# Kernel tuning notes

Hardware: AMD Instinct MI355X
Metric: run time of the kernel (lower is better)

The kernel has to match this reference:

```python
import jax, jax.numpy as jnp
import numpy as np

B, T, C, HS = 8, 4096, 1024, 128
BLOCK = 4096  # block_size; T == BLOCK here


def _pyr_mask(bs):
    # Faithful numpy translation of the torch 'pyr' buffer construction.
    h = bs // 2
    top = np.repeat(np.flip(np.tril(np.ones((h, h), np.float32)), axis=1), 2, axis=0)  # (bs, h)
    reps = np.array([2] * (h - 1) + [1])
    bot = np.concatenate(
        [np.zeros((1, h), np.float32),
         np.repeat(np.tril(np.ones((h, h), np.float32)), reps, axis=0)], axis=0)  # (bs, h)
    return np.concatenate([top, bot], axis=1)  # (bs, bs)


def setup_inputs() -> dict:
    key = jax.random.key(0)
    kx, kq, kk, kv = jax.random.split(key, 4)
    s = C ** -0.5
    x = jax.random.normal(kx, (B, T, C), jnp.float32)
    Wq = jax.random.normal(kq, (C, HS), jnp.float32) * s
    Wk = jax.random.normal(kk, (C, HS), jnp.float32) * s
    Wv = jax.random.normal(kv, (C, HS), jnp.float32) * s
    return {"x": x, "Wq": Wq, "Wk": Wk, "Wv": Wv}


def reference(x, Wq, Wk, Wv):
    Tlen = x.shape[1]
    start = (BLOCK - Tlen) // 2
    end = BLOCK + (-(BLOCK - Tlen)) // 2  # python floor-div, matches torch slicing
    mask = jnp.asarray(_pyr_mask(BLOCK)[:Tlen, start:end])  # (T, T) 0/1

    q = x @ Wq  # (B, T, HS)
    k = x @ Wk
    v = x @ Wv
    wei = jnp.einsum('btd,bsd->bts', q, k) * (HS ** -0.5)  # (B, T, T)
    wei = jnp.where(mask == 0, -jnp.inf, wei)  # bidirectional_mode == 'bi'
    wei = jax.nn.softmax(wei, axis=-1)
    # dropout p=0.0 -> identity
    return wei @ v  # (B, T, HS)
```

## Files before the change

kernel.cpp:

```cpp
#include <hip/hip_runtime.h>

typedef unsigned short u16;
typedef __attribute__((ext_vector_type(8))) short bf16x8;
typedef __attribute__((ext_vector_type(8))) unsigned short u16x8;
typedef __attribute__((ext_vector_type(4))) float f32x4;
typedef __attribute__((ext_vector_type(4))) unsigned short u16x4;
typedef __attribute__((ext_vector_type(2))) unsigned int u32x2;
typedef __attribute__((ext_vector_type(4))) unsigned int u32x4;

#define Bn 8
#define Tn 4096
#define Cn 1024
#define HSn 128

#define SBAR __builtin_amdgcn_sched_barrier(0)

__device__ __forceinline__ float bf2f(u16 b) {
    unsigned u = ((unsigned)b) << 16;
    return __builtin_bit_cast(float, u);
}
__device__ __forceinline__ unsigned cvt_pk_bf16(float a, float b) {
    unsigned r;
    asm("v_cvt_pk_bf16_f32 %0, %1, %2" : "=v"(r) : "v"(a), "v"(b));
    return r;
}
__device__ __forceinline__ u16 f2bf(float f) { return (u16)cvt_pk_bf16(f, f); }

__device__ __forceinline__ void wg_barrier() {
    __builtin_amdgcn_sched_barrier(0);
    asm volatile("s_waitcnt lgkmcnt(0)" ::: "memory");
    __builtin_amdgcn_s_barrier();
    __builtin_amdgcn_sched_barrier(0);
}

__device__ __forceinline__ void dma16(const void* g, void* l) {
    __builtin_amdgcn_global_load_lds(
        (const __attribute__((address_space(1))) unsigned int*)g,
        (__attribute__((address_space(3))) unsigned int*)l, 16, 0, 0);
}

extern "C" __global__ __launch_bounds__(256) void head_wtrans(
    const float* __restrict__ Wq, const float* __restrict__ Wk,
    const float* __restrict__ Wv, u16* __restrict__ wt) {
    const float* W = (blockIdx.y == 0) ? Wq : (blockIdx.y == 1) ? Wk : Wv;
    const float scale =
        (blockIdx.y == 0) ? (0.08838834764831845f * 1.4426950408889634f) : 1.0f;
    u16* o = wt + (size_t)blockIdx.y * Cn * HSn;
    int tid = blockIdx.x * 256 + threadIdx.x;
    int n = tid >> 10, kk = tid & 1023;
    o[tid] = f2bf(W[kk * HSn + n] * scale);
}

extern "C" __global__ __launch_bounds__(256) void head_proj(
    const float* __restrict__ x, const u16* __restrict__ wt, u16* __restrict__ qo,
    u16* __restrict__ ko, u16* __restrict__ vto) {
    __shared__ __align__(16) unsigned char sh[3 * 8192];
    const int tid = threadIdx.x;
    const int w = tid >> 6, l = tid & 63, quad = l >> 4, ln = l & 15;
    const int bm0 = blockIdx.x * 64;
    const int n0 = w * 96;

    const f32x4 zero4 = {0.f, 0.f, 0.f, 0.f};
    f32x4 acc[4][6];
#pragma unroll
    for (int fi = 0; fi < 4; fi++)
#pragma unroll
        for (int ci = 0; ci < 6; ci++) acc[fi][ci] = zero4;

    const float* xg[2];
    int xd[2];
#pragma unroll
    for (int p = 0; p < 2; p++) {
        int s = p * 256 + tid;
        int row = s >> 3, slot = s & 7;
        int g = slot ^ (row & 7);
        xg[p] = x + (size_t)(bm0 + row) * Cn + g * 4;
        xd[p] = s * 16;
    }
    int aoff[4];
#pragma unroll
    for (int fi = 0; fi < 4; fi++) {
        int row = fi * 16 + ln;
        aoff[fi] = row * 128 + (((2 * quad) ^ (row & 7)) * 16);
    }
    const u16* bp[6];
#pragma unroll
    for (int ci = 0; ci < 6; ci++)
        bp[ci] = wt + (size_t)(n0 + ci * 16 + ln) * Cn + quad * 8;

#define P_DMA(BUF, KT)                                       \
    do {                                                     \
        dma16(xg[0] + (KT) * 32, sh + (BUF) * 8192 + xd[0]); \
        dma16(xg[1] + (KT) * 32, sh + (BUF) * 8192 + xd[1]); \
    } while (0)

#define P_LOADB(DST, KT)                                   \
    do {                                                   \
        _Pragma("unroll") for (int ci = 0; ci < 6; ci++)   \
            DST[ci] = *(const u16x8*)(bp[ci] + (KT) * 32); \
    } while (0)

#define P_COMPUTE(BUF, BREG)                                               \
    do {                                                                   \
        const unsigned char* cb = sh + (BUF) * 8192;                       \
        bf16x8 af[4];                                                      \
        _Pragma("unroll") for (int fi = 0; fi < 4; fi++) {                 \
            f32x4 lo = *(const f32x4*)(cb + aoff[fi]);                     \
            f32x4 hi = *(const f32x4*)(cb + (aoff[fi] ^ 16));              \
            u32x4 tt;                                                      \
            tt[0] = cvt_pk_bf16(lo[0], lo[1]);                             \
            tt[1] = cvt_pk_bf16(lo[2], lo[3]);                             \
            tt[2] = cvt_pk_bf16(hi[0], hi[1]);                             \
            tt[3] = cvt_pk_bf16(hi[2], hi[3]);                             \
            af[fi] = __builtin_bit_cast(bf16x8, tt);                       \
        }                                                                  \
        _Pragma("unroll") for (int ci = 0; ci < 6; ci++) {                 \
            bf16x8 bfr = __builtin_bit_cast(bf16x8, BREG[ci]);             \
            _Pragma("unroll") for (int fi = 0; fi < 4; fi++)               \
                acc[fi][ci] = __builtin_amdgcn_mfma_f32_16x16x32_bf16(     \
                    af[fi], bfr, acc[fi][ci], 0, 0, 0);                    \
        }                                                                  \
    } while (0)

#define P_PHASE(T, BUF, BCUR, BNXT)                                         \
    do {                                                                    \
        int t_ = (T);                                                       \
        if (t_ < 32) {                                                      \
            P_COMPUTE(BUF, BCUR);                                           \
            wg_barrier();                                                   \
            if (t_ + 2 < 32) P_LOADB(BNXT, t_ + 2);                         \
            if (t_ + 3 < 32) P_DMA(BUF, t_ + 3);                            \
            SBAR;                                                           \
            if (t_ <= 28)                                                   \
                asm volatile("s_waitcnt vmcnt(16)" ::: "memory");           \
            else if (t_ == 29)                                              \
                asm volatile("s_waitcnt vmcnt(14)" ::: "memory");           \
            else if (t_ == 30)                                              \
                asm volatile("s_waitcnt vmcnt(6)" ::: "memory");            \
            if (t_ < 31) __builtin_amdgcn_s_barrier();                      \
            SBAR;                                                           \
        }                                                                   \
    } while (0)

    u16x8 b0[6], b1[6], b2[6];
    P_DMA(0, 0);
    P_LOADB(b0, 0);
    P_DMA(1, 1);
    P_LOADB(b1, 1);
    P_DMA(2, 2);
    SBAR;
    asm volatile("s_waitcnt vmcnt(16)" ::: "memory");
    __builtin_amdgcn_s_barrier();
    SBAR;

    for (int t3 = 0; t3 < 33; t3 += 3) {
        P_PHASE(t3 + 0, 0, b0, b2);
        P_PHASE(t3 + 1, 1, b1, b0);
        P_PHASE(t3 + 2, 2, b2, b1);
    }
#undef P_DMA
#undef P_LOADB
#undef P_COMPUTE
#undef P_PHASE

    u16* const tL = (u16*)sh;
#pragma unroll
    for (int ci = 0; ci < 6; ci++) {
        int col = n0 + ci * 16 + ln;
        int cin = col & 127;
        int sidx = col >> 7;
#pragma unroll
        for (int fi = 0; fi < 4; fi++) {
            int grow = bm0 + fi * 16 + quad * 4;
            if (sidx == 0) {
#pragma unroll
                for (int r = 0; r < 4; r++)
                    qo[(size_t)(grow + r) * HSn + cin] = f2bf(acc[fi][ci][r]);
            } else if (sidx == 1) {
#pragma unroll
                for (int r = 0; r < 4; r++)
                    ko[(size_t)(grow + r) * HSn + cin] = f2bf(acc[fi][ci][r]);
            } else {
                u16x4 pk4;
#pragma unroll
                for (int r = 0; r < 4; r++) pk4[r] = f2bf(acc[fi][ci][r]);
                *(u16x4*)(tL + cin * 80 + (fi * 16 + quad * 4)) = pk4;
            }
        }
    }
    wg_barrier();
    {
        const int bb = bm0 >> 12, t0b = bm0 & 4095;
        const int dl = tid >> 3, tch = (tid & 7) * 8;
#pragma unroll
        for (int dp = 0; dp < 4; dp++) {
            int d = dp * 32 + dl;
            u16x8 vv = *(const u16x8*)(tL + d * 80 + tch);
            *(u16x8*)(vto + ((size_t)bb * HSn + d) * Tn + t0b + tch) = vv;
        }
    }
}

extern "C" __global__ __launch_bounds__(512) void head_flash_chunk(
    const u16* __restrict__ q, const u16* __restrict__ k, const u16* __restrict__ vt,
    u16* __restrict__ Opart, float* __restrict__ lsum) {
    __shared__ __align__(16) u16 kL[64 * 136];
    __shared__ __align__(16) u16 vL[128 * 72];
    __shared__ __align__(16) u16 pL[8 * 16 * 72];
    const int tid = threadIdx.x;
    const int w = tid >> 6, l = tid & 63, quad = l >> 4, ln = l & 15;
    const int cid = blockIdx.x;
    const int grp = cid >> 4;
    const int qbi = (grp < 16) ? (31 - grp) : (grp - 16);
    const int b = (cid >> 1) & 7;
    const int half = cid & 1;
    const int q0 = qbi * 128;
    const int qrow = q0 + w * 16;

    const int rkBase = tid >> 4, ckK = tid & 15;
    const int rvBase = tid >> 3, ckV = tid & 7;

    bf16x8 qf[4];
#pragma unroll
    for (int ks = 0; ks < 4; ks++)
        qf[ks] = *(const bf16x8*)(q + ((size_t)b * Tn + qrow + ln) * HSn + ks * 32 +
                                  quad * 8);

    const f32x4 zero4 = {0.f, 0.f, 0.f, 0.f};
    float l2 = 0.f;
    const int qme = qrow + ln;
    const int clo = 2047 - (qme >> 1), chi = 2047 + ((qme + 1) >> 1);
    const int cloW0 = 2047 - (qrow >> 1);
    const int chiW0 = 2047 + ((qrow + 1) >> 1);
    const int cloMin = 2047 - ((qrow + 15) >> 1);
    const int chiMax = 2047 + ((qrow + 16) >> 1);
    f32x4 o[8];
#pragma unroll
    for (int dt = 0; dt < 8; dt++) o[dt] = zero4;

    const int qmax = q0 + 127;
    const int tlo = (2047 - (qmax >> 1)) >> 6;
    const int thi = (2047 + ((qmax + 1) >> 1)) >> 6;
    const int W = thi - tlo + 1;
    const int c0 = (W + 1) >> 1;
    const int kstart = half ? tlo + c0 : tlo;
    const int kend = half ? thi : tlo + c0 - 1;

    u16x8 pk[2], pv[2];
    {
        const int t0 = kstart * 64;
#pragma unroll
        for (int p = 0; p < 2; p++)
            pk[p] = *(const u16x8*)(k + ((size_t)b * Tn + t0 + p * 32 + rkBase) * HSn +
                                    ckK * 8);
#pragma unroll
        for (int p = 0; p < 2; p++)
            pv[p] = *(const u16x8*)(vt + ((size_t)b * HSn + p * 64 + rvBase) * Tn + t0 +
                                    ckV * 8);
    }

    for (int kt = kstart; kt <= kend; kt++) {
        const int t0 = kt * 64;
        wg_barrier();
#pragma unroll
        for (int p = 0; p < 2; p++)
            *(u16x8*)(kL + (p * 32 + rkBase) * 136 + ckK * 8) = pk[p];
#pragma unroll
        for (int p = 0; p < 2; p++)
            *(u16x8*)(vL + (p * 64 + rvBase) * 72 + ckV * 8) = pv[p];
        if (kt < kend) {
            const int t1 = t0 + 64;
#pragma unroll
            for (int p = 0; p < 2; p++)
                pk[p] = *(const u16x8*)(k + ((size_t)b * Tn + t1 + p * 32 + rkBase) * HSn +
                                        ckK * 8);
#pragma unroll
            for (int p = 0; p < 2; p++)
                pv[p] = *(const u16x8*)(vt + ((size_t)b * HSn + p * 64 + rvBase) * Tn +
                                        t1 + ckV * 8);
        }
        wg_barrier();

        const bool live = !((t0 + 63 < cloMin) || (t0 > chiMax));

        if (live) {
            f32x4 s[4];
#pragma unroll
            for (int nt = 0; nt < 4; nt++) s[nt] = zero4;
            __builtin_amdgcn_s_setprio(1);
#pragma unroll
            for (int nt = 0; nt < 4; nt++) {
                int R = nt * 16 + ln;
#pragma unroll
                for (int ks = 0; ks < 4; ks++) {
                    bf16x8 kf = *(const bf16x8*)(kL + R * 136 + (ks * 4 + quad) * 8);
                    s[nt] =
                        __builtin_amdgcn_mfma_f32_16x16x32_bf16(kf, qf[ks], s[nt], 0, 0, 0);
                }
            }
            __builtin_amdgcn_s_setprio(0);
            if (t0 < cloW0 || t0 + 63 > chiW0) {
#pragma unroll
                for (int nt = 0; nt < 4; nt++)
#pragma unroll
                    for (int r = 0; r < 4; r++) {
                        int t = t0 + nt * 16 + quad * 4 + r;
                        bool valid = (t >= clo) && (t <= chi);
                        s[nt][r] = valid ? s[nt][r] : -1e30f;
                    }
            }
            float ls = 0.f;
#pragma unroll
            for (int nt = 0; nt < 4; nt++) {
                float p0 = exp2f(s[nt][0]), p1 = exp2f(s[nt][1]);
                float p2 = exp2f(s[nt][2]), p3 = exp2f(s[nt][3]);
                ls += (p0 + p1) + (p2 + p3);
                u32x2 d;
                d.x = cvt_pk_bf16(p0, p1);
                d.y = cvt_pk_bf16(p2, p3);
                *(u32x2*)(pL + w * 1152 + ln * 72 + nt * 16 + quad * 4) = d;
            }
            l2 += ls;
            __builtin_amdgcn_s_setprio(1);
#pragma unroll
            for (int jt = 0; jt < 2; jt++) {
                bf16x8 pf = *(const bf16x8*)(pL + w * 1152 + ln * 72 + jt * 32 + quad * 8);
#pragma unroll
                for (int dt = 0; dt < 8; dt++) {
                    int R = dt * 16 + ln;
                    bf16x8 vf = *(const bf16x8*)(vL + R * 72 + (jt * 4 + quad) * 8);
                    o[dt] = __builtin_amdgcn_mfma_f32_16x16x32_bf16(pf, vf, o[dt], 0, 0, 0);
                }
            }
            __builtin_amdgcn_s_setprio(0);
        }
    }
    l2 += __shfl_xor(l2, 16, 64);
    l2 += __shfl_xor(l2, 32, 64);
#pragma unroll
    for (int dt = 0; dt < 8; dt++)
#pragma unroll
        for (int r = 0; r < 4; r++)
            Opart[((size_t)cid * 128 + w * 16 + quad * 4 + r) * HSn + dt * 16 + ln] =
                f2bf(o[dt][r]);
    if (l < 16) lsum[(size_t)cid * 128 + w * 16 + ln] = l2;
}

extern "C" __global__ __launch_bounds__(256) void head_combine(
    const u16* __restrict__ Opart, const float* __restrict__ lsum,
    float* __restrict__ out) {
    const int bid = blockIdx.x;
    const int qb64 = bid >> 3, b = bid & 7;
    const int tid = threadIdx.x;
    const int row = tid >> 2, dseg = (tid & 3) * 32;
    const int qbi = qb64 >> 1;
    const int inrow = (qb64 & 1) * 64 + row;
    const int grp0 = (qbi >= 16) ? (31 - qbi) : (qbi + 16);
    const int cid0 = grp0 * 16 + b * 2;
    const size_t r0 = (size_t)cid0 * 128 + inrow, r1 = r0 + 128;
    float l0 = lsum[r0], l1 = lsum[r1];
    float inv = 1.0f / (l0 + l1);
    float* op = out + ((size_t)b * Tn + qb64 * 64 + row) * HSn + dseg;
    const u16* p0 = Opart + r0 * HSn + dseg;
    const u16* p1 = Opart + r1 * HSn + dseg;
#pragma unroll
    for (int j = 0; j < 4; j++) {
        u16x8 a = *(const u16x8*)(p0 + j * 8);
        u16x8 c = *(const u16x8*)(p1 + j * 8);
        f32x4 o1, o2;
#pragma unroll
        for (int e = 0; e < 4; e++) o1[e] = (bf2f(a[e]) + bf2f(c[e])) * inv;
#pragma unroll
        for (int e = 0; e < 4; e++) o2[e] = (bf2f(a[4 + e]) + bf2f(c[4 + e])) * inv;
        *(f32x4*)(op + j * 8) = o1;
        *(f32x4*)(op + j * 8 + 4) = o2;
    }
}

extern "C" __global__ __launch_bounds__(256) void head_flash(
    const u16* __restrict__ q, const u16* __restrict__ k, const u16* __restrict__ vt,
    float* __restrict__ out) {
    __shared__ __align__(16) u16 kL[64 * 136];
    __shared__ __align__(16) u16 vL[128 * 72];
    __shared__ __align__(16) u16 pL[4 * 16 * 72];
    const int tid = threadIdx.x;
    const int w = tid >> 6, l = tid & 63, quad = l >> 4, ln = l & 15;
    const int bx = blockIdx.x;
    const int half = bx >> 8, idx = bx & 255;
    const int p5 = idx & 31, b = idx >> 5;
    const int qb = half ? p5 : 63 - p5;
    const int q0 = qb * 64;
    const int qrow = q0 + w * 16;
    const int rkBase = tid >> 4, ckK = tid & 15;
    const int rvBase = tid >> 3, ckV = tid & 7;

    bf16x8 qf[4];
#pragma unroll
    for (int ks = 0; ks < 4; ks++)
        qf[ks] = *(const bf16x8*)(q + ((size_t)b * Tn + qrow + ln) * HSn + ks * 32 +
                                  quad * 8);
    const f32x4 zero4 = {0.f, 0.f, 0.f, 0.f};
    float m2 = -1e30f, l2 = 0.f;
    const int qme = qrow + ln;
    const int clo = 2047 - (qme >> 1), chi = 2047 + ((qme + 1) >> 1);
    f32x4 o[8];
#pragma unroll
    for (int dt = 0; dt < 8; dt++) o[dt] = zero4;
    const int qmax = q0 + 63;
    const int tlo = (2047 - (qmax >> 1)) >> 6;
    const int thi = (2047 + ((qmax + 1) >> 1)) >> 6;

    u16x8 pk[4], pv[4];
    {
        const int t0 = tlo * 64;
#pragma unroll
        for (int p = 0; p < 4; p++)
            pk[p] = *(const u16x8*)(k + ((size_t)b * Tn + t0 + p * 16 + rkBase) * HSn +
                                    ckK * 8);
#pragma unroll
        for (int p = 0; p < 4; p++)
            pv[p] = *(const u16x8*)(vt + ((size_t)b * HSn + p * 32 + rvBase) * Tn + t0 +
                                    ckV * 8);
    }
    for (int kt = tlo; kt <= thi; kt++) {
        const int t0 = kt * 64;
        __syncthreads();
#pragma unroll
        for (int p = 0; p < 4; p++)
            *(u16x8*)(kL + (p * 16 + rkBase) * 136 + ckK * 8) = pk[p];
#pragma unroll
        for (int p = 0; p < 4; p++)
            *(u16x8*)(vL + (p * 32 + rvBase) * 72 + ckV * 8) = pv[p];
        if (kt < thi) {
            const int t1 = t0 + 64;
#pragma unroll
            for (int p = 0; p < 4; p++)
                pk[p] = *(const u16x8*)(k + ((size_t)b * Tn + t1 + p * 16 + rkBase) * HSn +
                                        ckK * 8);
#pragma unroll
            for (int p = 0; p < 4; p++)
                pv[p] = *(const u16x8*)(vt + ((size_t)b * HSn + p * 32 + rvBase) * Tn +
                                        t1 + ckV * 8);
        }
        __syncthreads();
        f32x4 s[4];
#pragma unroll
        for (int nt = 0; nt < 4; nt++) s[nt] = zero4;
#pragma unroll
        for (int nt = 0; nt < 4; nt++) {
            int R = nt * 16 + ln;
#pragma unroll
            for (int ks = 0; ks < 4; ks++) {
                bf16x8 kf = *(const bf16x8*)(kL + R * 136 + (ks * 4 + quad) * 8);
                s[nt] = __builtin_amdgcn_mfma_f32_16x16x32_bf16(kf, qf[ks], s[nt], 0, 0, 0);
            }
        }
#pragma unroll
        for (int nt = 0; nt < 4; nt++)
#pragma unroll
            for (int r = 0; r < 4; r++) {
                int t = t0 + nt * 16 + quad * 4 + r;
                bool valid = (t >= clo) && (t <= chi);
                s[nt][r] = valid ? s[nt][r] : -1e30f;
            }
        float mc = s[0][0];
#pragma unroll
        for (int nt = 0; nt < 4; nt++)
#pragma unroll
            for (int r = 0; r < 4; r++) mc = fmaxf(mc, s[nt][r]);
        mc = fmaxf(mc, __shfl_xor(mc, 16, 64));
        mc = fmaxf(mc, __shfl_xor(mc, 32, 64));
        float mn = fmaxf(m2, mc);
        float alpha = exp2f(m2 - mn);
        m2 = mn;
        float ls = 0.f;
#pragma unroll
        for (int nt = 0; nt < 4; nt++) {
            float p0 = exp2f(s[nt][0] - mn), p1 = exp2f(s[nt][1] - mn);
            float p2 = exp2f(s[nt][2] - mn), p3 = exp2f(s[nt][3] - mn);
            ls += (p0 + p1) + (p2 + p3);
            u32x2 d;
            d.x = cvt_pk_bf16(p0, p1);
            d.y = cvt_pk_bf16(p2, p3);
            *(u32x2*)(pL + w * 1152 + ln * 72 + nt * 16 + quad * 4) = d;
        }
        ls += __shfl_xor(ls, 16, 64);
        ls += __shfl_xor(ls, 32, 64);
        l2 = l2 * alpha + ls;
        float aR[4];
#pragma unroll
        for (int r = 0; r < 4; r++) aR[r] = __shfl(alpha, quad * 4 + r, 64);
#pragma unroll
        for (int dt = 0; dt < 8; dt++) {
            f32x4 oo = o[dt];
#pragma unroll
            for (int r = 0; r < 4; r++) oo[r] *= aR[r];
            o[dt] = oo;
        }
#pragma unroll
        for (int jt = 0; jt < 2; jt++) {
            bf16x8 pf = *(const bf16x8*)(pL + w * 1152 + ln * 72 + jt * 32 + quad * 8);
#pragma unroll
            for (int dt = 0; dt < 8; dt++) {
                int R = dt * 16 + ln;
                bf16x8 vf = *(const bf16x8*)(vL + R * 72 + (jt * 4 + quad) * 8);
                o[dt] = __builtin_amdgcn_mfma_f32_16x16x32_bf16(pf, vf, o[dt], 0, 0, 0);
            }
        }
    }
    float inv = 1.0f / l2;
    float rl[4];
#pragma unroll
    for (int r = 0; r < 4; r++) rl[r] = __shfl(inv, quad * 4 + r, 64);
#pragma unroll
    for (int dt = 0; dt < 8; dt++)
#pragma unroll
        for (int r = 0; r < 4; r++) {
            int row = qrow + quad * 4 + r;
            out[((size_t)b * Tn + row) * HSn + dt * 16 + ln] = o[dt][r] * rl[r];
        }
}

extern "C" void kernel_launch(void* const* d_in, const int* in_sizes, int n_in,
                              void* d_out, int out_size, void* d_ws, size_t ws_size,
                              hipStream_t stream) {
    const float* x = (const float*)d_in[0];
    const float* Wq = (const float*)d_in[1];
    const float* Wk = (const float*)d_in[2];
    const float* Wv = (const float*)d_in[3];
    float* outp = (float*)d_out;
    char* ws = (char*)d_ws;
    u16* wt = (u16*)(ws);
    u16* qb = (u16*)(ws + (1u << 20));
    u16* kb = (u16*)(ws + (9u << 20));
    u16* vtb = (u16*)(ws + (17u << 20));
    u16* Opart = (u16*)(ws + (25u << 20));
    float* lsum = (float*)(ws + (42u << 20));

    head_wtrans<<<dim3(512, 3), 256, 0, stream>>>(Wq, Wk, Wv, wt);
    head_proj<<<dim3(512), 256, 0, stream>>>(x, wt, qb, kb, vtb);
    if (ws_size >= (44ull << 20)) {
        head_flash_chunk<<<dim3(512), 512, 0, stream>>>(qb, kb, vtb, Opart, lsum);
        head_combine<<<dim3(512), 256, 0, stream>>>(Opart, lsum, outp);
    } else {
        head_flash<<<dim3(512), 256, 0, stream>>>(qb, kb, vtb, outp);
    }
}
```

Measured before the change: 310.5 us.

## Restructure projection GEMM pipeline to double buffering with asm loads and setprio

```diff
diff --git a/kernel.cpp b/kernel.cpp
--- a/kernel.cpp
+++ b/kernel.cpp
@@ -25,6 +25,12 @@
     return r;
 }
 __device__ __forceinline__ u16 f2bf(float f) { return (u16)cvt_pk_bf16(f, f); }
+
+__device__ __forceinline__ u32x4 gld16(const u16* p) {
+    u32x4 d;
+    asm volatile("global_load_dwordx4 %0, %1, off" : "=&v"(d) : "v"(p));
+    return d;
+}
 
 __device__ __forceinline__ void wg_barrier() {
     __builtin_amdgcn_sched_barrier(0);
@@ -54,7 +60,7 @@
 extern "C" __global__ __launch_bounds__(256) void head_proj(
     const float* __restrict__ x, const u16* __restrict__ wt, u16* __restrict__ qo,
     u16* __restrict__ ko, u16* __restrict__ vto) {
-    __shared__ __align__(16) unsigned char sh[3 * 8192];
+    __shared__ __align__(16) unsigned char sh[20480];
     const int tid = threadIdx.x;
     const int w = tid >> 6, l = tid & 63, quad = l >> 4, ln = l & 15;
     const int bm0 = blockIdx.x * 64;
@@ -94,10 +100,10 @@
         dma16(xg[1] + (KT) * 32, sh + (BUF) * 8192 + xd[1]); \
     } while (0)
 
-#define P_LOADB(DST, KT)                                   \
-    do {                                                   \
-        _Pragma("unroll") for (int ci = 0; ci < 6; ci++)   \
-            DST[ci] = *(const u16x8*)(bp[ci] + (KT) * 32); \
+#define P_LOADB(DST, KT)                                 \
+    do {                                                 \
+        _Pragma("unroll") for (int ci = 0; ci < 6; ci++) \
+            DST[ci] = gld16(bp[ci] + (KT) * 32);         \
     } while (0)
 
 #define P_COMPUTE(BUF, BREG)                                               \
@@ -114,55 +120,61 @@
             tt[3] = cvt_pk_bf16(hi[2], hi[3]);                             \
             af[fi] = __builtin_bit_cast(bf16x8, tt);                       \
         }                                                                  \
+        __builtin_amdgcn_s_setprio(1);                                     \
         _Pragma("unroll") for (int ci = 0; ci < 6; ci++) {                 \
             bf16x8 bfr = __builtin_bit_cast(bf16x8, BREG[ci]);             \
             _Pragma("unroll") for (int fi = 0; fi < 4; fi++)               \
                 acc[fi][ci] = __builtin_amdgcn_mfma_f32_16x16x32_bf16(     \
                     af[fi], bfr, acc[fi][ci], 0, 0, 0);                    \
         }                                                                  \
+        __builtin_amdgcn_s_setprio(0);                                     \
     } while (0)
 
-#define P_PHASE(T, BUF, BCUR, BNXT)                                         \
-    do {                                                                    \
-        int t_ = (T);                                                       \
-        if (t_ < 32) {                                                      \
-            P_COMPUTE(BUF, BCUR);                                           \
-            wg_barrier();                                                   \
-            if (t_ + 2 < 32) P_LOADB(BNXT, t_ + 2);                         \
-            if (t_ + 3 < 32) P_DMA(BUF, t_ + 3);                            \
-            SBAR;                                                           \
-            if (t_ <= 28)                                                   \
-                asm volatile("s_waitcnt vmcnt(16)" ::: "memory");           \
-            else if (t_ == 29)                                              \
-                asm volatile("s_waitcnt vmcnt(14)" ::: "memory");           \
-            else if (t_ == 30)                                              \
-                asm volatile("s_waitcnt vmcnt(6)" ::: "memory");            \
-            if (t_ < 31) __builtin_amdgcn_s_barrier();                      \
-            SBAR;                                                           \
-        }                                                                   \
+#define P_SYNC(ISSUED)                                              \
+    do {                                                            \
+        SBAR;                                                       \
+        if (ISSUED)                                                 \
+            asm volatile("s_waitcnt vmcnt(8)" ::: "memory");        \
+        else                                                        \
+            asm volatile("s_waitcnt vmcnt(0)" ::: "memory");        \
+        __builtin_amdgcn_s_barrier();                               \
+        SBAR;                                                       \
     } while (0)
 
-    u16x8 b0[6], b1[6], b2[6];
+    u32x4 bA[6], bB[6];
     P_DMA(0, 0);
-    P_LOADB(b0, 0);
+    P_LOADB(bA, 0);
     P_DMA(1, 1);
-    P_LOADB(b1, 1);
-    P_DMA(2, 2);
+    P_LOADB(bB, 1);
     SBAR;
-    asm volatile("s_waitcnt vmcnt(16)" ::: "memory");
+    asm volatile("s_waitcnt vmcnt(8)" ::: "memory");
     __builtin_amdgcn_s_barrier();
     SBAR;
 
-    for (int t3 = 0; t3 < 33; t3 += 3) {
-        P_PHASE(t3 + 0, 0, b0, b2);
-        P_PHASE(t3 + 1, 1, b1, b0);
-        P_PHASE(t3 + 2, 2, b2, b1);
+    for (int t = 0; t < 32; t += 2) {
+        P_COMPUTE(0, bA);
+        wg_barrier();
+        if (t + 2 < 32) {
+            P_DMA(0, t + 2);
+            P_LOADB(bA, t + 2);
+        }
+        P_SYNC(t + 2 < 32);
+        P_COMPUTE(1, bB);
+        if (t + 1 < 31) {
+            wg_barrier();
+            if (t + 3 < 32) {
+                P_DMA(1, t + 3);
+                P_LOADB(bB, t + 3);
+            }
+            P_SYNC(t + 3 < 32);
+        }
     }
 #undef P_DMA
 #undef P_LOADB
 #undef P_COMPUTE
-#undef P_PHASE
-
+#undef P_SYNC
+
+    wg_barrier();
     u16* const tL = (u16*)sh;
 #pragma unroll
     for (int ci = 0; ci < 6; ci++) {
```

Measured after the change: 312.9 us. About the same (+0.8%).
